# Kernel optimization log

Measured on AMD Instinct MI355X. Metric: run time of the kernel, lower is better.

## Reference

```python
import jax, jax.numpy as jnp
import numpy as np

N = 768      # n_proto (number of class prototypes)
D = 128      # trans_feat_num
H = D // 16  # edge-MLP hidden = 8
A = 312      # semantic attribute dim
INIT_TEMP = 0.1
VTEMP = 10.0
STEMP = 10.0
EPS = 1e-8


def _layer_norm(x, g, b, eps=1e-5):
    m = x.mean(-1, keepdims=True)
    v = ((x - m) ** 2).mean(-1, keepdims=True)
    return (x - m) / jnp.sqrt(v + eps) * g + b


def _instance_norm_rows(x, eps=1e-5):
    # torch InstanceNorm1d on 2D input: unbatched (C, L) -> normalize each row, no affine
    m = x.mean(-1, keepdims=True)
    v = ((x - m) ** 2).mean(-1, keepdims=True)
    return (x - m) / jnp.sqrt(v + eps)


def _init_edge(x, temp):
    # pairwise cosine similarity + row softmax
    nrm = jnp.linalg.norm(x, axis=1)
    sim = (x @ x.T) / jnp.maximum(nrm[:, None] * nrm[None, :], EPS)
    return jax.nn.softmax(sim / temp, axis=-1)


def _edge_update(proto, last_edge, W1, b1, W2, b2, temp):
    n, d = proto.shape
    # O(n^2) pairwise squared differences  -> [n*n, d]
    feat = ((proto[:, None, :] - proto[None, :, :]) ** 2).reshape(n * n, d)
    h = jax.nn.relu(_instance_norm_rows(feat @ W1.T + b1))  # [n*n, H]
    e = jnp.tanh(h @ W2.T + b2).reshape(n, n)
    return jax.nn.softmax(e * (last_edge + EPS) / temp, axis=-1)


def _node_update(proto, last_edge, edge, W, b, g, beta):
    extra = last_edge @ proto          # cross-modal message (dist_injection)
    p = edge @ proto                   # same-modal aggregation
    return jax.nn.relu(_layer_norm((p + extra) @ W.T + b, g, beta)) + p


def setup_inputs() -> dict:
    key = jax.random.key(0)
    ks = jax.random.split(key, 9)
    rn = lambda k, shape, s=1.0: jax.random.normal(k, shape, dtype=jnp.float32) * s
    return {
        "visual_proto": rn(ks[0], (N, D)),
        "semantic_proto": rn(ks[1], (N, D)),
        "attribute": rn(ks[2], (N, A)),
        "Wvn": rn(ks[3], (D, D), 0.08), "bvn": jnp.zeros((D,), jnp.float32),
        "gvn": jnp.ones((D,), jnp.float32), "betavn": jnp.zeros((D,), jnp.float32),
        "Wve1": rn(ks[4], (H, D), 0.1), "bve1": jnp.zeros((H,), jnp.float32),
        "Wve2": rn(ks[5], (1, H), 0.3), "bve2": jnp.zeros((1,), jnp.float32),
        "Wsn": rn(ks[6], (D, D), 0.08), "bsn": jnp.zeros((D,), jnp.float32),
        "gsn": jnp.ones((D,), jnp.float32), "betasn": jnp.zeros((D,), jnp.float32),
        "Wse1": rn(ks[7], (H, D), 0.1), "bse1": jnp.zeros((H,), jnp.float32),
        "Wse2": rn(ks[8], (1, H), 0.3), "bse2": jnp.zeros((1,), jnp.float32),
    }


def reference(visual_proto, semantic_proto, attribute,
              Wvn, bvn, gvn, betavn, Wve1, bve1, Wve2, bve2,
              Wsn, bsn, gsn, betasn, Wse1, bse1, Wse2, bse2):
    ve = _init_edge(visual_proto, INIT_TEMP)
    se = _init_edge(attribute, INIT_TEMP)
    vp = _node_update(visual_proto, se, ve, Wvn, bvn, gvn, betavn)
    ve2 = _edge_update(vp, ve, Wve1, bve1, Wve2, bve2, VTEMP)
    sp = _node_update(semantic_proto, ve2, se, Wsn, bsn, gsn, betasn)
    se2 = _edge_update(sp, se, Wse1, bse1, Wse2, bse2, STEMP)
    return vp, sp, ve2, se2
```

## Files before the change

### kernel.cpp

```cpp
#include <hip/hip_runtime.h>
#include <math.h>

#define NN 768
#define DD 128
#define AA 312
#define HH 8
#define CEPS 1e-8f

typedef __attribute__((ext_vector_type(8))) short s8b;
typedef __attribute__((ext_vector_type(4))) float f4v;

__device__ __forceinline__ float wave_sum(float v) {
    #pragma unroll
    for (int o = 32; o; o >>= 1) v += __shfl_down(v, o, 64);
    return v;
}
__device__ __forceinline__ float wave_max(float v) {
    #pragma unroll
    for (int o = 32; o; o >>= 1) v = fmaxf(v, __shfl_down(v, o, 64));
    return v;
}
__device__ __forceinline__ unsigned short f2bf(float f) {
    unsigned u = __float_as_uint(f);
    u += 0x7FFFu + ((u >> 16) & 1u);
    return (unsigned short)(u >> 16);
}

struct KParams {
    const float *visual, *semantic, *attribute;
    const float *Wvn, *bvn, *gvn, *betavn, *Wve1, *bve1, *Wve2, *bve2;
    const float *Wsn, *bsn, *gsn, *betasn, *Wse1, *bse1, *Wse2, *bse2;
    float *vp, *sp, *ve2, *se2;
    float *simv, *sima, *WvnT, *WsnT, *cvec1, *cvec2;
    float *nrmv, *nrma, *ve, *se;
    short *vpb, *spb;
};

__global__ __launch_bounds__(256) void gram_mfma_kernel(KParams p) {
    __shared__ __align__(16) unsigned short AH[64 * 40];
    __shared__ __align__(16) unsigned short AL[64 * 40];
    __shared__ __align__(16) unsigned short BH[64 * 40];
    __shared__ __align__(16) unsigned short BL[64 * 40];
    const int task = blockIdx.x;
    const int tid = threadIdx.x;
    if (task < 288) {
        const bool isv = (task < 144);
        const int tt = isv ? task : task - 144;
        const int bi = tt / 12, bj = tt % 12;
        const float* M = isv ? p.visual : p.attribute;
        float* G = isv ? p.simv : p.sima;
        float* nrm = isv ? p.nrmv : p.nrma;
        const int K = isv ? DD : AA;
        const int i0 = bi * 64, j0 = bj * 64;
        const int w = tid >> 6, lane = tid & 63;
        const int m = lane & 15, q = lane >> 4;
        f4v acc[4] = {{0.f, 0.f, 0.f, 0.f}, {0.f, 0.f, 0.f, 0.f},
                      {0.f, 0.f, 0.f, 0.f}, {0.f, 0.f, 0.f, 0.f}};
        const int nchunk = (K + 31) >> 5;
        const int srow = tid >> 2, sq = (tid & 3) * 8;
        for (int c = 0; c < nchunk; ++c) {
            const int kc = c * 32;
            __syncthreads();
            #pragma unroll
            for (int h = 0; h < 2; ++h) {
                const int col = sq + h * 4;
                float4 a = {0.f, 0.f, 0.f, 0.f}, b = {0.f, 0.f, 0.f, 0.f};
                if (kc + col + 4 <= K) {
                    a = *(const float4*)(M + (size_t)(i0 + srow) * K + kc + col);
                    b = *(const float4*)(M + (size_t)(j0 + srow) * K + kc + col);
                }
                const float av[4] = {a.x, a.y, a.z, a.w};
                const float bv[4] = {b.x, b.y, b.z, b.w};
                #pragma unroll
                for (int e = 0; e < 4; ++e) {
                    const unsigned short ah = f2bf(av[e]);
                    const float ahf = __uint_as_float((unsigned)ah << 16);
                    const unsigned short al = f2bf(av[e] - ahf);
                    const unsigned short bh = f2bf(bv[e]);
                    const float bhf = __uint_as_float((unsigned)bh << 16);
                    const unsigned short bl = f2bf(bv[e] - bhf);
                    AH[srow * 40 + col + e] = ah;
                    AL[srow * 40 + col + e] = al;
                    BH[srow * 40 + col + e] = bh;
                    BL[srow * 40 + col + e] = bl;
                }
            }
            __syncthreads();
            const s8b ah8 = *(const s8b*)&AH[(w * 16 + m) * 40 + q * 8];
            const s8b al8 = *(const s8b*)&AL[(w * 16 + m) * 40 + q * 8];
            #pragma unroll
            for (int jt = 0; jt < 4; ++jt) {
                const s8b bh8 = *(const s8b*)&BH[(jt * 16 + m) * 40 + q * 8];
                const s8b bl8 = *(const s8b*)&BL[(jt * 16 + m) * 40 + q * 8];
                acc[jt] = __builtin_amdgcn_mfma_f32_16x16x32_bf16(ah8, bh8, acc[jt], 0, 0, 0);
                acc[jt] = __builtin_amdgcn_mfma_f32_16x16x32_bf16(ah8, bl8, acc[jt], 0, 0, 0);
                acc[jt] = __builtin_amdgcn_mfma_f32_16x16x32_bf16(al8, bh8, acc[jt], 0, 0, 0);
            }
        }
        #pragma unroll
        for (int jt = 0; jt < 4; ++jt) {
            #pragma unroll
            for (int r = 0; r < 4; ++r) {
                G[(size_t)(i0 + w * 16 + q * 4 + r) * NN + j0 + jt * 16 + m] = acc[jt][r];
                if (bi == bj && jt == w && m == q * 4 + r)
                    nrm[i0 + w * 16 + m] = sqrtf(fmaxf(acc[jt][r], 0.f));
            }
        }
    } else {
        float* smem = (float*)AH;
        const int u = task - 288;
        const float* S = (u >= 16) ? p.Wsn : p.Wvn;
        float* Dt = (u >= 16) ? p.WsnT : p.WvnT;
        const int tile = u & 15;
        const int c0 = (tile & 3) * 32, r0 = (tile >> 2) * 32;
        const int tx = tid & 31, ty = tid >> 5;
        #pragma unroll
        for (int rr = ty; rr < 32; rr += 8)
            smem[rr * 33 + tx] = S[(size_t)(r0 + rr) * DD + c0 + tx];
        __syncthreads();
        #pragma unroll
        for (int rr = ty; rr < 32; rr += 8)
            Dt[(size_t)(c0 + rr) * DD + r0 + tx] = smem[tx * 33 + rr];
    }
}

__device__ void softmax768_pair(float* A, float* B, int tid, float* red) {
    float* buf = (tid < 256) ? A : B;
    const int st = tid & 255;
    const int g = tid >> 8;
    const int w4 = (tid >> 6) & 3;
    float v0 = buf[st], v1 = buf[st + 256], v2 = buf[st + 512];
    float m = wave_max(fmaxf(fmaxf(v0, v1), v2));
    if ((tid & 63) == 0) red[g * 8 + w4] = m;
    __syncthreads();
    m = fmaxf(fmaxf(red[g * 8], red[g * 8 + 1]), fmaxf(red[g * 8 + 2], red[g * 8 + 3]));
    float e0 = __expf(v0 - m), e1 = __expf(v1 - m), e2 = __expf(v2 - m);
    float sw = wave_sum(e0 + e1 + e2);
    if ((tid & 63) == 0) red[g * 8 + 4 + w4] = sw;
    __syncthreads();
    const float s = red[g * 8 + 4] + red[g * 8 + 5] + red[g * 8 + 6] + red[g * 8 + 7];
    const float inv = 1.f / s;
    buf[st] = e0 * inv;
    buf[st + 256] = e1 * inv;
    buf[st + 512] = e2 * inv;
    __syncthreads();
}

__device__ void norm_rows(float (*buf)[NN], const float* __restrict__ nrm, int i0, int tid) {
    const float n0 = nrm[i0], n1 = nrm[i0 + 1];
    for (int k = tid; k < NN; k += 512) {
        const float nj = nrm[k];
        buf[0][k] = buf[0][k] * 10.f / fmaxf(n0 * nj, CEPS);
        buf[1][k] = buf[1][k] * 10.f / fmaxf(n1 * nj, CEPS);
    }
}

__device__ void node_core(const float* __restrict__ P, float (*ep)[NN], float (*ex)[NN],
                          const float* __restrict__ WT, const float* __restrict__ b,
                          const float* __restrict__ g, const float* __restrict__ beta,
                          float* __restrict__ out, const float* __restrict__ W1e,
                          short* __restrict__ outb, float* __restrict__ cvec, int i0, int tid,
                          float* ppart, float* xpart, float (*qs)[DD], float (*tps)[2][DD],
                          float* red) {
    {
        const int kg = tid >> 6, dp = tid & 63, d0 = dp * 2;
        const float2* P2 = (const float2*)P;
        float a00 = 0.f, a01 = 0.f, a10 = 0.f, a11 = 0.f;
        float b00 = 0.f, b01 = 0.f, b10 = 0.f, b11 = 0.f;
        const int kb = kg * 96;
        #pragma unroll 8
        for (int i = 0; i < 96; ++i) {
            const int k = kb + i;
            const float2 pv = P2[(size_t)k * 64 + dp];
            const float e0 = ep[0][k], e1 = ep[1][k];
            const float f0 = ex[0][k], f1 = ex[1][k];
            a00 = fmaf(e0, pv.x, a00); a01 = fmaf(e0, pv.y, a01);
            a10 = fmaf(e1, pv.x, a10); a11 = fmaf(e1, pv.y, a11);
            b00 = fmaf(f0, pv.x, b00); b01 = fmaf(f0, pv.y, b01);
            b10 = fmaf(f1, pv.x, b10); b11 = fmaf(f1, pv.y, b11);
        }
        float* pp = ppart + kg * 260;
        float* xp = xpart + kg * 260;
        pp[d0] = a00; pp[d0 + 1] = a01; pp[130 + d0] = a10; pp[130 + d0 + 1] = a11;
        xp[d0] = b00; xp[d0 + 1] = b01; xp[130 + d0] = b10; xp[130 + d0 + 1] = b11;
    }
    __syncthreads();
    const int rr = (tid >> 7) & 1, d = tid & 127;
    float preg = 0.f;
    if (tid < 256) {
        float p = 0.f, x = 0.f;
        #pragma unroll
        for (int kk = 0; kk < 8; ++kk) {
            p += ppart[kk * 260 + rr * 130 + d];
            x += xpart[kk * 260 + rr * 130 + d];
        }
        qs[rr][d] = p + x;
        preg = p;
    }
    __syncthreads();
    {
        const int sc = tid >> 8, rr2 = (tid >> 7) & 1;
        float t = (sc == 0) ? b[d] : 0.f;
        const int c0 = sc * 64;
        #pragma unroll 4
        for (int c = c0; c < c0 + 64; ++c) t = fmaf(qs[rr2][c], WT[(size_t)c * DD + d], t);
        tps[sc][rr2][d] = t;
    }
    __syncthreads();
    float tval = 0.f;
    if (tid < 256) tval = tps[0][rr][d] + tps[1][rr][d];
    float sm = wave_sum(tid < 256 ? tval : 0.f);
    if ((tid & 63) == 0) red[tid >> 6] = sm;
    __syncthreads();
    if (tid < 256) tval -= (red[2 * rr] + red[2 * rr + 1]) * (1.f / DD);
    float s2 = wave_sum(tid < 256 ? tval * tval : 0.f);
    if ((tid & 63) == 0) red[8 + (tid >> 6)] = s2;
    __syncthreads();
    if (tid < 256) {
        const float var = (red[8 + 2 * rr] + red[8 + 2 * rr + 1]) * (1.f / DD);
        const float ln = tval * rsqrtf(var + 1e-5f) * g[d] + beta[d];
        const float val = fmaxf(ln, 0.f) + preg;
        out[(size_t)(i0 + rr) * DD + d] = val;
        outb[(size_t)(i0 + rr) * DD + d] = (short)f2bf(val);
        qs[rr][d] = val;
    }
    __syncthreads();
    if (tid < 256) {
        const int row = tid >> 7, r = (tid >> 4) & 7, l16 = tid & 15;
        float ssum = 0.f;
        #pragma unroll
        for (int t = 0; t < 8; ++t) {
            const int k = l16 + 16 * t;
            const float pv = qs[row][k];
            ssum = fmaf(W1e[r * DD + k], pv * pv, ssum);
        }
        #pragma unroll
        for (int o = 8; o; o >>= 1) ssum += __shfl_down(ssum, o, 16);
        if (l16 == 0) cvec[(size_t)(i0 + row) * HH + r] = ssum;
    }
}

__global__ __launch_bounds__(512) void node1_kernel(KParams p) {
    __shared__ __align__(16) float ep[2][NN], ex[2][NN];
    __shared__ __align__(16) float ppart[8 * 260], xpart[8 * 260];
    __shared__ __align__(16) float qs[2][DD], tps[2][2][DD];
    __shared__ float red[16];
    const int i0 = blockIdx.x * 2;
    const int tid = threadIdx.x;
    if (tid < 384) {
        ((float4*)ep)[tid] = ((const float4*)(p.simv + (size_t)i0 * NN))[tid];
        ((float4*)ex)[tid] = ((const float4*)(p.sima + (size_t)i0 * NN))[tid];
    }
    __syncthreads();
    norm_rows(ep, p.nrmv, i0, tid);
    norm_rows(ex, p.nrma, i0, tid);
    __syncthreads();
    softmax768_pair(ep[0], ex[0], tid, red);
    softmax768_pair(ep[1], ex[1], tid, red);
    if (tid < 384) {
        ((float4*)(p.ve + (size_t)i0 * NN))[tid] = ((float4*)ep)[tid];
        ((float4*)(p.se + (size_t)i0 * NN))[tid] = ((float4*)ex)[tid];
    }
    node_core(p.visual, ep, ex, p.WvnT, p.bvn, p.gvn, p.betavn, p.vp, p.Wve1, p.vpb, p.cvec1,
              i0, tid, ppart, xpart, qs, tps, red);
}

__device__ void edge_core(const short* __restrict__ PRb, const float* __restrict__ cvec,
                          const float* __restrict__ W1, const float* __restrict__ b1,
                          const float* __restrict__ W2, const float* __restrict__ b2,
                          float invtemp, int i0, int tid, float (*pi)[DD], float* w1s,
                          short* a_sw, float (*Lv)[NN], float (*Ls)[NN]) {
    const int lane = tid & 63, wave = tid >> 6;
    if (tid < 256) {
        const int t = tid >> 6, m = lane & 15, q2 = lane >> 4;
        const int il = m >> 3, r = m & 7;
        const int kb = t * 32 + q2 * 8;
        s8b av;
        #pragma unroll
        for (int e = 0; e < 8; ++e)
            av[e] = (short)f2bf(pi[il][kb + e] * w1s[r * DD + kb + e]);
        *(s8b*)&a_sw[(t * 64 + lane) * 8] = av;
    }
    __syncthreads();
    s8b af[4];
    #pragma unroll
    for (int t = 0; t < 4; ++t) af[t] = *(const s8b*)&a_sw[(t * 64 + lane) * 8];
    const int q = lane >> 4, n = lane & 15;
    const int rbase = (q & 1) * 4;
    const int il = q >> 1;
    const float4 ci4 = *(const float4*)&cvec[(size_t)(i0 + il) * HH + rbase];
    const float4 b14 = *(const float4*)&b1[rbase];
    const float4 w24 = *(const float4*)&W2[rbase];
    const float b2s = b2[0];
    #pragma unroll
    for (int s = 0; s < 6; ++s) {
        const int j = wave * 96 + s * 16 + n;
        f4v acc = {0.f, 0.f, 0.f, 0.f};
        #pragma unroll
        for (int t = 0; t < 4; ++t) {
            const s8b bf = *(const s8b*)(PRb + (size_t)j * DD + t * 32 + q * 8);
            acc = __builtin_amdgcn_mfma_f32_16x16x32_bf16(af[t], bf, acc, 0, 0, 0);
        }
        const float4 cj = *(const float4*)&cvec[(size_t)j * HH + rbase];
        float z[4];
        z[0] = ci4.x + cj.x - 2.f * acc[0] + b14.x;
        z[1] = ci4.y + cj.y - 2.f * acc[1] + b14.y;
        z[2] = ci4.z + cj.z - 2.f * acc[2] + b14.z;
        z[3] = ci4.w + cj.w - 2.f * acc[3] + b14.w;
        float s1 = z[0] + z[1] + z[2] + z[3];
        float s2 = z[0] * z[0] + z[1] * z[1] + z[2] * z[2] + z[3] * z[3];
        s1 += __shfl_xor(s1, 16, 64);
        s2 += __shfl_xor(s2, 16, 64);
        const float mean = s1 * (1.f / HH);
        const float var = fmaxf(s2 * (1.f / HH) - mean * mean, 0.f);
        const float istd = rsqrtf(var + 1e-5f);
        float a2 = 0.f;
        a2 = fmaf(fmaxf((z[0] - mean) * istd, 0.f), w24.x, a2);
        a2 = fmaf(fmaxf((z[1] - mean) * istd, 0.f), w24.y, a2);
        a2 = fmaf(fmaxf((z[2] - mean) * istd, 0.f), w24.z, a2);
        a2 = fmaf(fmaxf((z[3] - mean) * istd, 0.f), w24.w, a2);
        a2 += __shfl_xor(a2, 16, 64);
        const float tv = tanhf(a2 + b2s);
        const float lv = Lv[il][j];
        if ((q & 1) == 0) Ls[il][j] = tv * (lv + CEPS) * invtemp;
    }
    __syncthreads();
}

__global__ __launch_bounds__(512) void edge_node_kernel(KParams p) {
    __shared__ __align__(16) float pi[2][DD];
    __shared__ __align__(16) float w1s[HH * DD];
    __shared__ __align__(16) short a_sw[4 * 64 * 8];
    __shared__ __align__(16) float Lv[2][NN];
    __shared__ __align__(16) float Ls[2][NN];
    __shared__ __align__(16) float ep[2][NN];
    __shared__ __align__(16) float ppart[8 * 260], xpart[8 * 260];
    __shared__ __align__(16) float qs[2][DD], tps[2][2][DD];
    __shared__ float red[16];
    const int i0 = blockIdx.x * 2;
    const int tid = threadIdx.x;
    if (tid < 256) {
        pi[tid >> 7][tid & 127] = p.vp[(size_t)(i0 + (tid >> 7)) * DD + (tid & 127)];
        ((float4*)w1s)[tid] = ((const float4*)p.Wve1)[tid];
    }
    if (tid < 384) {
        ((float4*)Lv)[tid] = ((const float4*)(p.ve + (size_t)i0 * NN))[tid];
        ((float4*)ep)[tid] = ((const float4*)(p.se + (size_t)i0 * NN))[tid];
    }
    __syncthreads();
    edge_core(p.vpb, p.cvec1, p.Wve1, p.bve1, p.Wve2, p.bve2, 0.1f, i0, tid, pi, w1s, a_sw,
              Lv, Ls);
    softmax768_pair(Ls[0], Ls[1], tid, red);
    if (tid < 384)
        ((float4*)(p.ve2 + (size_t)i0 * NN))[tid] = ((float4*)Ls)[tid];
    node_core(p.semantic, ep, Ls, p.WsnT, p.bsn, p.gsn, p.betasn, p.sp, p.Wse1, p.spb,
              p.cvec2, i0, tid, ppart, xpart, qs, tps, red);
}

__global__ __launch_bounds__(512) void edge2_kernel(KParams p) {
    __shared__ __align__(16) float pi[2][DD];
    __shared__ __align__(16) float w1s[HH * DD];
    __shared__ __align__(16) short a_sw[4 * 64 * 8];
    __shared__ __align__(16) float Lv[2][NN];
    __shared__ __align__(16) float Ls[2][NN];
    __shared__ float red[16];
    const int i0 = blockIdx.x * 2;
    const int tid = threadIdx.x;
    if (tid < 256) {
        pi[tid >> 7][tid & 127] = p.sp[(size_t)(i0 + (tid >> 7)) * DD + (tid & 127)];
        ((float4*)w1s)[tid] = ((const float4*)p.Wse1)[tid];
    }
    if (tid < 384)
        ((float4*)Lv)[tid] = ((const float4*)(p.se + (size_t)i0 * NN))[tid];
    __syncthreads();
    edge_core(p.spb, p.cvec2, p.Wse1, p.bse1, p.Wse2, p.bse2, 0.1f, i0, tid, pi, w1s, a_sw,
              Lv, Ls);
    softmax768_pair(Ls[0], Ls[1], tid, red);
    float* d0 = p.se2 + (size_t)i0 * NN;
    float* d1 = p.se2 + (size_t)(i0 + 1) * NN;
    d0[tid] = Ls[0][tid];
    d1[tid] = Ls[1][tid];
    if (tid < NN - 512) {
        d0[tid + 512] = Ls[0][tid + 512];
        d1[tid + 512] = Ls[1][tid + 512];
    }
}

extern "C" void kernel_launch(void* const* d_in, const int* in_sizes, int n_in, void* d_out,
                              int out_size, void* d_ws, size_t ws_size, hipStream_t stream) {
    KParams kp;
    kp.visual    = (const float*)d_in[0];
    kp.semantic  = (const float*)d_in[1];
    kp.attribute = (const float*)d_in[2];
    kp.Wvn  = (const float*)d_in[3];
    kp.bvn  = (const float*)d_in[4];
    kp.gvn  = (const float*)d_in[5];
    kp.betavn = (const float*)d_in[6];
    kp.Wve1 = (const float*)d_in[7];
    kp.bve1 = (const float*)d_in[8];
    kp.Wve2 = (const float*)d_in[9];
    kp.bve2 = (const float*)d_in[10];
    kp.Wsn  = (const float*)d_in[11];
    kp.bsn  = (const float*)d_in[12];
    kp.gsn  = (const float*)d_in[13];
    kp.betasn = (const float*)d_in[14];
    kp.Wse1 = (const float*)d_in[15];
    kp.bse1 = (const float*)d_in[16];
    kp.Wse2 = (const float*)d_in[17];
    kp.bse2 = (const float*)d_in[18];

    float* out = (float*)d_out;
    kp.vp  = out;
    kp.sp  = out + 98304;
    kp.ve2 = out + 196608;
    kp.se2 = out + 786432;

    float* ws = (float*)d_ws;
    kp.simv  = ws;
    kp.sima  = ws + 589824;
    kp.ve    = ws + 1179648;
    kp.se    = ws + 1769472;
    kp.WvnT  = ws + 2949120;
    kp.WsnT  = ws + 2965504;
    kp.cvec1 = ws + 2981888;
    kp.cvec2 = ws + 2988032;
    kp.vpb   = (short*)(ws + 2994176);
    kp.spb   = (short*)(ws + 3043328);
    kp.nrmv  = ws + 3092480;
    kp.nrma  = ws + 3093248;

    gram_mfma_kernel<<<320, 256, 0, stream>>>(kp);
    node1_kernel<<<NN / 2, 512, 0, stream>>>(kp);
    edge_node_kernel<<<NN / 2, 512, 0, stream>>>(kp);
    edge2_kernel<<<NN / 2, 512, 0, stream>>>(kp);
}
```

Measured before the change: 176.9 us.

## Process one row per block instead of two across node and edge kernels

Each block of the three row-wise kernels now handles a single row rather than a pair, which doubles the grid to 768 blocks. The Wx matvec split goes from 2 to 4 chunks, and a single-row block softmax is added. The aim is more blocks in flight and less shared memory per block, for better occupancy across the 256 CUs. The cost is that each block reads the P matrix and weights again, since they are no longer reused across two rows. Half of the MFMA A-tile rows are also zero-padded, which wastes matrix throughput in the edge kernel.

New measurement: 201.0 us. +13.6%, slower.

```diff
diff --git a/kernel.cpp b/kernel.cpp
--- a/kernel.cpp
+++ b/kernel.cpp
@@ -146,139 +146,150 @@
     __syncthreads();
 }
 
-__device__ void norm_rows(float (*buf)[NN], const float* __restrict__ nrm, int i0, int tid) {
-    const float n0 = nrm[i0], n1 = nrm[i0 + 1];
-    for (int k = tid; k < NN; k += 512) {
-        const float nj = nrm[k];
-        buf[0][k] = buf[0][k] * 10.f / fmaxf(n0 * nj, CEPS);
-        buf[1][k] = buf[1][k] * 10.f / fmaxf(n1 * nj, CEPS);
-    }
-}
-
-__device__ void node_core(const float* __restrict__ P, float (*ep)[NN], float (*ex)[NN],
-                          const float* __restrict__ WT, const float* __restrict__ b,
-                          const float* __restrict__ g, const float* __restrict__ beta,
-                          float* __restrict__ out, const float* __restrict__ W1e,
-                          short* __restrict__ outb, float* __restrict__ cvec, int i0, int tid,
-                          float* ppart, float* xpart, float (*qs)[DD], float (*tps)[2][DD],
-                          float* red) {
+__device__ void block_softmax768(float* buf, int tid, float* red) {
+    const int w = tid >> 6, lane = tid & 63;
+    float v0 = buf[tid];
+    float v1 = (tid < NN - 512) ? buf[tid + 512] : -3.4e38f;
+    float m = wave_max(fmaxf(v0, v1));
+    if (lane == 0) red[w] = m;
+    __syncthreads();
+    m = red[0];
+    #pragma unroll
+    for (int i = 1; i < 8; ++i) m = fmaxf(m, red[i]);
+    float e0 = __expf(v0 - m);
+    float e1 = (tid < NN - 512) ? __expf(v1 - m) : 0.f;
+    float sw = wave_sum(e0 + e1);
+    if (lane == 0) red[8 + w] = sw;
+    __syncthreads();
+    float s = 0.f;
+    #pragma unroll
+    for (int i = 0; i < 8; ++i) s += red[8 + i];
+    const float inv = 1.f / s;
+    buf[tid] = e0 * inv;
+    if (tid < NN - 512) buf[tid + 512] = e1 * inv;
+    __syncthreads();
+}
+
+__device__ void node_core1(const float* __restrict__ P, float* ep, float* ex,
+                           const float* __restrict__ WT, const float* __restrict__ b,
+                           const float* __restrict__ g, const float* __restrict__ beta,
+                           float* __restrict__ out, const float* __restrict__ W1e,
+                           short* __restrict__ outb, float* __restrict__ cvec, int i, int tid,
+                           float* ppart, float* xpart, float* qs, float (*tps)[DD],
+                           float* red) {
     {
         const int kg = tid >> 6, dp = tid & 63, d0 = dp * 2;
         const float2* P2 = (const float2*)P;
-        float a00 = 0.f, a01 = 0.f, a10 = 0.f, a11 = 0.f;
-        float b00 = 0.f, b01 = 0.f, b10 = 0.f, b11 = 0.f;
+        float a0 = 0.f, a1 = 0.f, b0 = 0.f, b1 = 0.f;
         const int kb = kg * 96;
         #pragma unroll 8
-        for (int i = 0; i < 96; ++i) {
-            const int k = kb + i;
+        for (int it = 0; it < 96; ++it) {
+            const int k = kb + it;
             const float2 pv = P2[(size_t)k * 64 + dp];
-            const float e0 = ep[0][k], e1 = ep[1][k];
-            const float f0 = ex[0][k], f1 = ex[1][k];
-            a00 = fmaf(e0, pv.x, a00); a01 = fmaf(e0, pv.y, a01);
-            a10 = fmaf(e1, pv.x, a10); a11 = fmaf(e1, pv.y, a11);
-            b00 = fmaf(f0, pv.x, b00); b01 = fmaf(f0, pv.y, b01);
-            b10 = fmaf(f1, pv.x, b10); b11 = fmaf(f1, pv.y, b11);
-        }
-        float* pp = ppart + kg * 260;
-        float* xp = xpart + kg * 260;
-        pp[d0] = a00; pp[d0 + 1] = a01; pp[130 + d0] = a10; pp[130 + d0 + 1] = a11;
-        xp[d0] = b00; xp[d0 + 1] = b01; xp[130 + d0] = b10; xp[130 + d0 + 1] = b11;
-    }
-    __syncthreads();
-    const int rr = (tid >> 7) & 1, d = tid & 127;
+            const float e0 = ep[k], f0 = ex[k];
+            a0 = fmaf(e0, pv.x, a0); a1 = fmaf(e0, pv.y, a1);
+            b0 = fmaf(f0, pv.x, b0); b1 = fmaf(f0, pv.y, b1);
+        }
+        ppart[kg * 130 + d0] = a0; ppart[kg * 130 + d0 + 1] = a1;
+        xpart[kg * 130 + d0] = b0; xpart[kg * 130 + d0 + 1] = b1;
+    }
+    __syncthreads();
+    const int d = tid & 127;
     float preg = 0.f;
-    if (tid < 256) {
-        float p = 0.f, x = 0.f;
+    if (tid < 128) {
+        float pv = 0.f, xv = 0.f;
         #pragma unroll
         for (int kk = 0; kk < 8; ++kk) {
-            p += ppart[kk * 260 + rr * 130 + d];
-            x += xpart[kk * 260 + rr * 130 + d];
-        }
-        qs[rr][d] = p + x;
-        preg = p;
+            pv += ppart[kk * 130 + d];
+            xv += xpart[kk * 130 + d];
+        }
+        qs[d] = pv + xv;
+        preg = pv;
     }
     __syncthreads();
     {
-        const int sc = tid >> 8, rr2 = (tid >> 7) & 1;
+        const int sc = tid >> 7;
         float t = (sc == 0) ? b[d] : 0.f;
-        const int c0 = sc * 64;
+        const int c0 = sc * 32;
         #pragma unroll 4
-        for (int c = c0; c < c0 + 64; ++c) t = fmaf(qs[rr2][c], WT[(size_t)c * DD + d], t);
-        tps[sc][rr2][d] = t;
+        for (int c = c0; c < c0 + 32; ++c) t = fmaf(qs[c], WT[(size_t)c * DD + d], t);
+        tps[sc][d] = t;
     }
     __syncthreads();
     float tval = 0.f;
-    if (tid < 256) tval = tps[0][rr][d] + tps[1][rr][d];
-    float sm = wave_sum(tid < 256 ? tval : 0.f);
-    if ((tid & 63) == 0) red[tid >> 6] = sm;
-    __syncthreads();
-    if (tid < 256) tval -= (red[2 * rr] + red[2 * rr + 1]) * (1.f / DD);
-    float s2 = wave_sum(tid < 256 ? tval * tval : 0.f);
-    if ((tid & 63) == 0) red[8 + (tid >> 6)] = s2;
-    __syncthreads();
-    if (tid < 256) {
-        const float var = (red[8 + 2 * rr] + red[8 + 2 * rr + 1]) * (1.f / DD);
+    if (tid < 128) tval = tps[0][d] + tps[1][d] + tps[2][d] + tps[3][d];
+    float sm = wave_sum(tid < 128 ? tval : 0.f);
+    if ((tid & 63) == 0 && tid < 128) red[tid >> 6] = sm;
+    __syncthreads();
+    if (tid < 128) tval -= (red[0] + red[1]) * (1.f / DD);
+    float s2 = wave_sum(tid < 128 ? tval * tval : 0.f);
+    if ((tid & 63) == 0 && tid < 128) red[8 + (tid >> 6)] = s2;
+    __syncthreads();
+    if (tid < 128) {
+        const float var = (red[8] + red[9]) * (1.f / DD);
         const float ln = tval * rsqrtf(var + 1e-5f) * g[d] + beta[d];
         const float val = fmaxf(ln, 0.f) + preg;
-        out[(size_t)(i0 + rr) * DD + d] = val;
-        outb[(size_t)(i0 + rr) * DD + d] = (short)f2bf(val);
-        qs[rr][d] = val;
-    }
-    __syncthreads();
-    if (tid < 256) {
-        const int row = tid >> 7, r = (tid >> 4) & 7, l16 = tid & 15;
+        out[(size_t)i * DD + d] = val;
+        outb[(size_t)i * DD + d] = (short)f2bf(val);
+        qs[d] = val;
+    }
+    __syncthreads();
+    if (tid < 128) {
+        const int r = tid >> 4, l16 = tid & 15;
         float ssum = 0.f;
         #pragma unroll
         for (int t = 0; t < 8; ++t) {
             const int k = l16 + 16 * t;
-            const float pv = qs[row][k];
+            const float pv = qs[k];
             ssum = fmaf(W1e[r * DD + k], pv * pv, ssum);
         }
         #pragma unroll
         for (int o = 8; o; o >>= 1) ssum += __shfl_down(ssum, o, 16);
-        if (l16 == 0) cvec[(size_t)(i0 + row) * HH + r] = ssum;
+        if (l16 == 0) cvec[(size_t)i * HH + r] = ssum;
     }
 }
 
 __global__ __launch_bounds__(512) void node1_kernel(KParams p) {
-    __shared__ __align__(16) float ep[2][NN], ex[2][NN];
-    __shared__ __align__(16) float ppart[8 * 260], xpart[8 * 260];
-    __shared__ __align__(16) float qs[2][DD], tps[2][2][DD];
+    __shared__ __align__(16) float ep[NN], ex[NN];
+    __shared__ __align__(16) float ppart[8 * 130], xpart[8 * 130];
+    __shared__ __align__(16) float qs[DD], tps[4][DD];
     __shared__ float red[16];
-    const int i0 = blockIdx.x * 2;
+    const int i = blockIdx.x;
     const int tid = threadIdx.x;
-    if (tid < 384) {
-        ((float4*)ep)[tid] = ((const float4*)(p.simv + (size_t)i0 * NN))[tid];
-        ((float4*)ex)[tid] = ((const float4*)(p.sima + (size_t)i0 * NN))[tid];
-    }
-    __syncthreads();
-    norm_rows(ep, p.nrmv, i0, tid);
-    norm_rows(ex, p.nrma, i0, tid);
-    __syncthreads();
-    softmax768_pair(ep[0], ex[0], tid, red);
-    softmax768_pair(ep[1], ex[1], tid, red);
-    if (tid < 384) {
-        ((float4*)(p.ve + (size_t)i0 * NN))[tid] = ((float4*)ep)[tid];
-        ((float4*)(p.se + (size_t)i0 * NN))[tid] = ((float4*)ex)[tid];
-    }
-    node_core(p.visual, ep, ex, p.WvnT, p.bvn, p.gvn, p.betavn, p.vp, p.Wve1, p.vpb, p.cvec1,
-              i0, tid, ppart, xpart, qs, tps, red);
-}
-
-__device__ void edge_core(const short* __restrict__ PRb, const float* __restrict__ cvec,
-                          const float* __restrict__ W1, const float* __restrict__ b1,
-                          const float* __restrict__ W2, const float* __restrict__ b2,
-                          float invtemp, int i0, int tid, float (*pi)[DD], float* w1s,
-                          short* a_sw, float (*Lv)[NN], float (*Ls)[NN]) {
+    if (tid < 192) ((float4*)ep)[tid] = ((const float4*)(p.simv + (size_t)i * NN))[tid];
+    else if (tid < 384) ((float4*)ex)[tid - 192] = ((const float4*)(p.sima + (size_t)i * NN))[tid - 192];
+    __syncthreads();
+    {
+        const float niv = p.nrmv[i], nia = p.nrma[i];
+        const int k0 = tid, k1 = tid + 512;
+        ep[k0] = ep[k0] * 10.f / fmaxf(niv * p.nrmv[k0], CEPS);
+        ex[k0] = ex[k0] * 10.f / fmaxf(nia * p.nrma[k0], CEPS);
+        if (k1 < NN) {
+            ep[k1] = ep[k1] * 10.f / fmaxf(niv * p.nrmv[k1], CEPS);
+            ex[k1] = ex[k1] * 10.f / fmaxf(nia * p.nrma[k1], CEPS);
+        }
+    }
+    __syncthreads();
+    softmax768_pair(ep, ex, tid, red);
+    if (tid < 192) ((float4*)(p.ve + (size_t)i * NN))[tid] = ((float4*)ep)[tid];
+    else if (tid < 384) ((float4*)(p.se + (size_t)i * NN))[tid - 192] = ((float4*)ex)[tid - 192];
+    node_core1(p.visual, ep, ex, p.WvnT, p.bvn, p.gvn, p.betavn, p.vp, p.Wve1, p.vpb, p.cvec1,
+               i, tid, ppart, xpart, qs, tps, red);
+}
+
+__device__ void edge_core1(const short* __restrict__ PRb, const float* __restrict__ cvec,
+                           const float* __restrict__ b1, const float* __restrict__ W2,
+                           const float* __restrict__ b2, float invtemp, int i, int tid,
+                           float* pi, float* w1s, short* a_sw, float* Lv, float* Ls) {
     const int lane = tid & 63, wave = tid >> 6;
     if (tid < 256) {
         const int t = tid >> 6, m = lane & 15, q2 = lane >> 4;
-        const int il = m >> 3, r = m & 7;
+        const int r = m & 7;
         const int kb = t * 32 + q2 * 8;
         s8b av;
         #pragma unroll
         for (int e = 0; e < 8; ++e)
-            av[e] = (short)f2bf(pi[il][kb + e] * w1s[r * DD + kb + e]);
+            av[e] = (m < 8) ? (short)f2bf(pi[kb + e] * w1s[r * DD + kb + e]) : (short)0;
         *(s8b*)&a_sw[(t * 64 + lane) * 8] = av;
     }
     __syncthreads();
@@ -287,8 +298,7 @@
     for (int t = 0; t < 4; ++t) af[t] = *(const s8b*)&a_sw[(t * 64 + lane) * 8];
     const int q = lane >> 4, n = lane & 15;
     const int rbase = (q & 1) * 4;
-    const int il = q >> 1;
-    const float4 ci4 = *(const float4*)&cvec[(size_t)(i0 + il) * HH + rbase];
+    const float4 ci4 = *(const float4*)&cvec[(size_t)i * HH + rbase];
     const float4 b14 = *(const float4*)&b1[rbase];
     const float4 w24 = *(const float4*)&W2[rbase];
     const float b2s = b2[0];
@@ -321,69 +331,51 @@
         a2 = fmaf(fmaxf((z[3] - mean) * istd, 0.f), w24.w, a2);
         a2 += __shfl_xor(a2, 16, 64);
         const float tv = tanhf(a2 + b2s);
-        const float lv = Lv[il][j];
-        if ((q & 1) == 0) Ls[il][j] = tv * (lv + CEPS) * invtemp;
+        const float lv = Lv[j];
+        if (q == 0) Ls[j] = tv * (lv + CEPS) * invtemp;
     }
     __syncthreads();
 }
 
 __global__ __launch_bounds__(512) void edge_node_kernel(KParams p) {
-    __shared__ __align__(16) float pi[2][DD];
+    __shared__ __align__(16) float pi[DD];
     __shared__ __align__(16) float w1s[HH * DD];
     __shared__ __align__(16) short a_sw[4 * 64 * 8];
-    __shared__ __align__(16) float Lv[2][NN];
-    __shared__ __align__(16) float Ls[2][NN];
-    __shared__ __align__(16) float ep[2][NN];
-    __shared__ __align__(16) float ppart[8 * 260], xpart[8 * 260];
-    __shared__ __align__(16) float qs[2][DD], tps[2][2][DD];
+    __shared__ __align__(16) float Lv[NN], Ls[NN], ep[NN];
+    __shared__ __align__(16) float ppart[8 * 130], xpart[8 * 130];
+    __shared__ __align__(16) float qs[DD], tps[4][DD];
     __shared__ float red[16];
-    const int i0 = blockIdx.x * 2;
+    const int i = blockIdx.x;
     const int tid = threadIdx.x;
-    if (tid < 256) {
-        pi[tid >> 7][tid & 127] = p.vp[(size_t)(i0 + (tid >> 7)) * DD + (tid & 127)];
-        ((float4*)w1s)[tid] = ((const float4*)p.Wve1)[tid];
-    }
-    if (tid < 384) {
-        ((float4*)Lv)[tid] = ((const float4*)(p.ve + (size_t)i0 * NN))[tid];
-        ((float4*)ep)[tid] = ((const float4*)(p.se + (size_t)i0 * NN))[tid];
-    }
-    __syncthreads();
-    edge_core(p.vpb, p.cvec1, p.Wve1, p.bve1, p.Wve2, p.bve2, 0.1f, i0, tid, pi, w1s, a_sw,
-              Lv, Ls);
-    softmax768_pair(Ls[0], Ls[1], tid, red);
-    if (tid < 384)
-        ((float4*)(p.ve2 + (size_t)i0 * NN))[tid] = ((float4*)Ls)[tid];
-    node_core(p.semantic, ep, Ls, p.WsnT, p.bsn, p.gsn, p.betasn, p.sp, p.Wse1, p.spb,
-              p.cvec2, i0, tid, ppart, xpart, qs, tps, red);
+    if (tid < 32) ((float4*)pi)[tid] = ((const float4*)(p.vp + (size_t)i * DD))[tid];
+    if (tid < 256) ((float4*)w1s)[tid] = ((const float4*)p.Wve1)[tid];
+    if (tid < 192) ((float4*)Lv)[tid] = ((const float4*)(p.ve + (size_t)i * NN))[tid];
+    else if (tid < 384) ((float4*)ep)[tid - 192] = ((const float4*)(p.se + (size_t)i * NN))[tid - 192];
+    __syncthreads();
+    edge_core1(p.vpb, p.cvec1, p.bve1, p.Wve2, p.bve2, 0.1f, i, tid, pi, w1s, a_sw, Lv, Ls);
+    block_softmax768(Ls, tid, red);
+    if (tid < 192) ((float4*)(p.ve2 + (size_t)i * NN))[tid] = ((float4*)Ls)[tid];
+    node_core1(p.semantic, ep, Ls, p.WsnT, p.bsn, p.gsn, p.betasn, p.sp, p.Wse1, p.spb,
+               p.cvec2, i, tid, ppart, xpart, qs, tps, red);
 }
 
 __global__ __launch_bounds__(512) void edge2_kernel(KParams p) {
-    __shared__ __align__(16) float pi[2][DD];
+    __shared__ __align__(16) float pi[DD];
     __shared__ __align__(16) float w1s[HH * DD];
     __shared__ __align__(16) short a_sw[4 * 64 * 8];
-    __shared__ __align__(16) float Lv[2][NN];
-    __shared__ __align__(16) float Ls[2][NN];
+    __shared__ __align__(16) float Lv[NN], Ls[NN];
     __shared__ float red[16];
-    const int i0 = blockIdx.x * 2;
+    const int i = blockIdx.x;
     const int tid = threadIdx.x;
-    if (tid < 256) {
-        pi[tid >> 7][tid & 127] = p.sp[(size_t)(i0 + (tid >> 7)) * DD + (tid & 127)];
-        ((float4*)w1s)[tid] = ((const float4*)p.Wse1)[tid];
-    }
-    if (tid < 384)
-        ((float4*)Lv)[tid] = ((const float4*)(p.se + (size_t)i0 * NN))[tid];
-    __syncthreads();
-    edge_core(p.spb, p.cvec2, p.Wse1, p.bse1, p.Wse2, p.bse2, 0.1f, i0, tid, pi, w1s, a_sw,
-              Lv, Ls);
-    softmax768_pair(Ls[0], Ls[1], tid, red);
-    float* d0 = p.se2 + (size_t)i0 * NN;
-    float* d1 = p.se2 + (size_t)(i0 + 1) * NN;
-    d0[tid] = Ls[0][tid];
-    d1[tid] = Ls[1][tid];
-    if (tid < NN - 512) {
-        d0[tid + 512] = Ls[0][tid + 512];
-        d1[tid + 512] = Ls[1][tid + 512];
-    }
+    if (tid < 32) ((float4*)pi)[tid] = ((const float4*)(p.sp + (size_t)i * DD))[tid];
+    if (tid < 256) ((float4*)w1s)[tid] = ((const float4*)p.Wse1)[tid];
+    if (tid < 192) ((float4*)Lv)[tid] = ((const float4*)(p.se + (size_t)i * NN))[tid];
+    __syncthreads();
+    edge_core1(p.spb, p.cvec2, p.bse1, p.Wse2, p.bse2, 0.1f, i, tid, pi, w1s, a_sw, Lv, Ls);
+    block_softmax768(Ls, tid, red);
+    float* d0 = p.se2 + (size_t)i * NN;
+    d0[tid] = Ls[tid];
+    if (tid < NN - 512) d0[tid + 512] = Ls[tid + 512];
 }
 
 extern "C" void kernel_launch(void* const* d_in, const int* in_sizes, int n_in, void* d_out,
@@ -430,7 +422,7 @@
     kp.nrma  = ws + 3093248;
 
     gram_mfma_kernel<<<320, 256, 0, stream>>>(kp);
-    node1_kernel<<<NN / 2, 512, 0, stream>>>(kp);
-    edge_node_kernel<<<NN / 2, 512, 0, stream>>>(kp);
-    edge2_kernel<<<NN / 2, 512, 0, stream>>>(kp);
-}
+    node1_kernel<<<NN, 512, 0, stream>>>(kp);
+    edge_node_kernel<<<NN, 512, 0, stream>>>(kp);
+    edge2_kernel<<<NN, 512, 0, stream>>>(kp);
+}
```

## Move edge@proto aggregations to split-bf16 MFMA GEMM kernels

Applied to the files above, without the earlier changes.

Replaces the per-row-pair FP32 FMA aggregation inside node kernels with separate MFMA GEMM kernels. Edge matrices are stored as hi/lo bf16 pairs and the prototypes as transposed bf16. The pipeline now has separate softmax, aggregation, tail (linear+layernorm) and edge kernels. The aim is to cut the scalar FMA cost of the 768x768x128 products. In exchange it adds launches, workspace traffic, and a GEMM grid of only 12 blocks, and it loses some precision because the prototypes are rounded to bf16.

Result: slower. 291.1 us (+64.5%).

```diff
diff --git a/kernel.cpp b/kernel.cpp
--- a/kernel.cpp
+++ b/kernel.cpp
@@ -33,7 +33,9 @@
     float *vp, *sp, *ve2, *se2;
     float *simv, *sima, *WvnT, *WsnT, *cvec1, *cvec2;
     float *nrmv, *nrma, *ve, *se;
-    short *vpb, *spb;
+    float *pagg1, *xagg1, *pagg2, *xagg2;
+    short *vpb, *spb, *visbT, *sembT;
+    short *veh, *vel, *seh, *sel, *ve2h, *ve2l;
 };
 
 __global__ __launch_bounds__(256) void gram_mfma_kernel(KParams p) {
@@ -106,7 +108,7 @@
                     nrm[i0 + w * 16 + m] = sqrtf(fmaxf(acc[jt][r], 0.f));
             }
         }
-    } else {
+    } else if (task < 320) {
         float* smem = (float*)AH;
         const int u = task - 288;
         const float* S = (u >= 16) ? p.Wsn : p.Wvn;
@@ -121,6 +123,21 @@
         #pragma unroll
         for (int rr = ty; rr < 32; rr += 8)
             Dt[(size_t)(c0 + rr) * DD + r0 + tx] = smem[tx * 33 + rr];
+    } else {
+        const int u = task - 320;
+        const bool isv = (u < 12);
+        const float* src = isv ? p.visual : p.semantic;
+        short* dst = isv ? p.visbT : p.sembT;
+        const int r0 = (isv ? u : u - 12) * 64;
+        for (int e = tid * 4; e < 8192; e += 1024) {
+            const int r = r0 + (e >> 7);
+            const int c = e & 127;
+            const float4 v = *(const float4*)(src + (size_t)r * DD + c);
+            dst[(size_t)(c + 0) * NN + r] = (short)f2bf(v.x);
+            dst[(size_t)(c + 1) * NN + r] = (short)f2bf(v.y);
+            dst[(size_t)(c + 2) * NN + r] = (short)f2bf(v.z);
+            dst[(size_t)(c + 3) * NN + r] = (short)f2bf(v.w);
+        }
     }
 }
 
@@ -155,47 +172,91 @@
     }
 }
 
-__device__ void node_core(const float* __restrict__ P, float (*ep)[NN], float (*ex)[NN],
-                          const float* __restrict__ WT, const float* __restrict__ b,
-                          const float* __restrict__ g, const float* __restrict__ beta,
-                          float* __restrict__ out, const float* __restrict__ W1e,
-                          short* __restrict__ outb, float* __restrict__ cvec, int i0, int tid,
-                          float* ppart, float* xpart, float (*qs)[DD], float (*tps)[2][DD],
-                          float* red) {
-    {
-        const int kg = tid >> 6, dp = tid & 63, d0 = dp * 2;
-        const float2* P2 = (const float2*)P;
-        float a00 = 0.f, a01 = 0.f, a10 = 0.f, a11 = 0.f;
-        float b00 = 0.f, b01 = 0.f, b10 = 0.f, b11 = 0.f;
-        const int kb = kg * 96;
-        #pragma unroll 8
-        for (int i = 0; i < 96; ++i) {
-            const int k = kb + i;
-            const float2 pv = P2[(size_t)k * 64 + dp];
-            const float e0 = ep[0][k], e1 = ep[1][k];
-            const float f0 = ex[0][k], f1 = ex[1][k];
-            a00 = fmaf(e0, pv.x, a00); a01 = fmaf(e0, pv.y, a01);
-            a10 = fmaf(e1, pv.x, a10); a11 = fmaf(e1, pv.y, a11);
-            b00 = fmaf(f0, pv.x, b00); b01 = fmaf(f0, pv.y, b01);
-            b10 = fmaf(f1, pv.x, b10); b11 = fmaf(f1, pv.y, b11);
-        }
-        float* pp = ppart + kg * 260;
-        float* xp = xpart + kg * 260;
-        pp[d0] = a00; pp[d0 + 1] = a01; pp[130 + d0] = a10; pp[130 + d0 + 1] = a11;
-        xp[d0] = b00; xp[d0 + 1] = b01; xp[130 + d0] = b10; xp[130 + d0 + 1] = b11;
-    }
-    __syncthreads();
+__global__ __launch_bounds__(512) void sm1_kernel(KParams p) {
+    __shared__ __align__(16) float ep[2][NN], ex[2][NN];
+    __shared__ float red[16];
+    const int i0 = blockIdx.x * 2;
+    const int tid = threadIdx.x;
+    if (tid < 384) {
+        ((float4*)ep)[tid] = ((const float4*)(p.simv + (size_t)i0 * NN))[tid];
+        ((float4*)ex)[tid] = ((const float4*)(p.sima + (size_t)i0 * NN))[tid];
+    }
+    __syncthreads();
+    norm_rows(ep, p.nrmv, i0, tid);
+    norm_rows(ex, p.nrma, i0, tid);
+    __syncthreads();
+    softmax768_pair(ep[0], ex[0], tid, red);
+    softmax768_pair(ep[1], ex[1], tid, red);
+    if (tid < 384) {
+        ((float4*)(p.ve + (size_t)i0 * NN))[tid] = ((float4*)ep)[tid];
+        ((float4*)(p.se + (size_t)i0 * NN))[tid] = ((float4*)ex)[tid];
+    }
+    #pragma unroll
+    for (int j = 0; j < 3; ++j) {
+        const int e = tid + j * 512;
+        const int row = e / NN, k = e - row * NN;
+        const size_t off = (size_t)(i0 + row) * NN + k;
+        float v = ep[row][k];
+        unsigned short h = f2bf(v);
+        p.veh[off] = (short)h;
+        p.vel[off] = (short)f2bf(v - __uint_as_float((unsigned)h << 16));
+        v = ex[row][k];
+        h = f2bf(v);
+        p.seh[off] = (short)h;
+        p.sel[off] = (short)f2bf(v - __uint_as_float((unsigned)h << 16));
+    }
+}
+
+__global__ __launch_bounds__(512) void agg_kernel(
+        const short* __restrict__ Eh, const short* __restrict__ El,
+        const short* __restrict__ Fh, const short* __restrict__ Fl,
+        const short* __restrict__ PT, float* __restrict__ Pagg, float* __restrict__ Xagg) {
+    const int tid = threadIdx.x, lane = tid & 63, wv = tid >> 6;
+    const int grp = wv >> 2, strip = wv & 3;
+    const short* Ah = grp ? Fh : Eh;
+    const short* Al = grp ? Fl : El;
+    float* Out = grp ? Xagg : Pagg;
+    const int m = lane & 15, q = lane >> 4;
+    const int arow = blockIdx.x * 64 + strip * 16 + m;
+    f4v acc[8] = {{0.f, 0.f, 0.f, 0.f}, {0.f, 0.f, 0.f, 0.f}, {0.f, 0.f, 0.f, 0.f},
+                  {0.f, 0.f, 0.f, 0.f}, {0.f, 0.f, 0.f, 0.f}, {0.f, 0.f, 0.f, 0.f},
+                  {0.f, 0.f, 0.f, 0.f}, {0.f, 0.f, 0.f, 0.f}};
+    for (int kb = 0; kb < NN; kb += 32) {
+        const s8b ah = *(const s8b*)(Ah + (size_t)arow * NN + kb + q * 8);
+        const s8b al = *(const s8b*)(Al + (size_t)arow * NN + kb + q * 8);
+        #pragma unroll
+        for (int nt = 0; nt < 8; ++nt) {
+            const s8b bf = *(const s8b*)(PT + (size_t)(nt * 16 + m) * NN + kb + q * 8);
+            acc[nt] = __builtin_amdgcn_mfma_f32_16x16x32_bf16(ah, bf, acc[nt], 0, 0, 0);
+            acc[nt] = __builtin_amdgcn_mfma_f32_16x16x32_bf16(al, bf, acc[nt], 0, 0, 0);
+        }
+    }
+    const int orow = blockIdx.x * 64 + strip * 16 + q * 4;
+    #pragma unroll
+    for (int nt = 0; nt < 8; ++nt) {
+        #pragma unroll
+        for (int r = 0; r < 4; ++r)
+            Out[(size_t)(orow + r) * DD + nt * 16 + m] = acc[nt][r];
+    }
+}
+
+__global__ __launch_bounds__(512) void tail_kernel(
+        const float* __restrict__ Pagg, const float* __restrict__ Xagg,
+        const float* __restrict__ WT, const float* __restrict__ b,
+        const float* __restrict__ g, const float* __restrict__ beta,
+        float* __restrict__ out, const float* __restrict__ W1e,
+        short* __restrict__ outb, float* __restrict__ cvec) {
+    __shared__ __align__(16) float qs[2][DD], tps[2][2][DD];
+    __shared__ float red[16];
+    const int i0 = blockIdx.x * 2;
+    const int tid = threadIdx.x;
     const int rr = (tid >> 7) & 1, d = tid & 127;
     float preg = 0.f;
     if (tid < 256) {
-        float p = 0.f, x = 0.f;
-        #pragma unroll
-        for (int kk = 0; kk < 8; ++kk) {
-            p += ppart[kk * 260 + rr * 130 + d];
-            x += xpart[kk * 260 + rr * 130 + d];
-        }
-        qs[rr][d] = p + x;
-        preg = p;
+        const float pv = Pagg[(size_t)(i0 + rr) * DD + d];
+        const float xv = Xagg[(size_t)(i0 + rr) * DD + d];
+        qs[rr][d] = pv + xv;
+        preg = pv;
     }
     __syncthreads();
     {
@@ -240,36 +301,11 @@
     }
 }
 
-__global__ __launch_bounds__(512) void node1_kernel(KParams p) {
-    __shared__ __align__(16) float ep[2][NN], ex[2][NN];
-    __shared__ __align__(16) float ppart[8 * 260], xpart[8 * 260];
-    __shared__ __align__(16) float qs[2][DD], tps[2][2][DD];
-    __shared__ float red[16];
-    const int i0 = blockIdx.x * 2;
-    const int tid = threadIdx.x;
-    if (tid < 384) {
-        ((float4*)ep)[tid] = ((const float4*)(p.simv + (size_t)i0 * NN))[tid];
-        ((float4*)ex)[tid] = ((const float4*)(p.sima + (size_t)i0 * NN))[tid];
-    }
-    __syncthreads();
-    norm_rows(ep, p.nrmv, i0, tid);
-    norm_rows(ex, p.nrma, i0, tid);
-    __syncthreads();
-    softmax768_pair(ep[0], ex[0], tid, red);
-    softmax768_pair(ep[1], ex[1], tid, red);
-    if (tid < 384) {
-        ((float4*)(p.ve + (size_t)i0 * NN))[tid] = ((float4*)ep)[tid];
-        ((float4*)(p.se + (size_t)i0 * NN))[tid] = ((float4*)ex)[tid];
-    }
-    node_core(p.visual, ep, ex, p.WvnT, p.bvn, p.gvn, p.betavn, p.vp, p.Wve1, p.vpb, p.cvec1,
-              i0, tid, ppart, xpart, qs, tps, red);
-}
-
 __device__ void edge_core(const short* __restrict__ PRb, const float* __restrict__ cvec,
-                          const float* __restrict__ W1, const float* __restrict__ b1,
-                          const float* __restrict__ W2, const float* __restrict__ b2,
-                          float invtemp, int i0, int tid, float (*pi)[DD], float* w1s,
-                          short* a_sw, float (*Lv)[NN], float (*Ls)[NN]) {
+                          const float* __restrict__ b1, const float* __restrict__ W2,
+                          const float* __restrict__ b2, float invtemp, int i0, int tid,
+                          float (*pi)[DD], float* w1s, short* a_sw, float (*Lv)[NN],
+                          float (*Ls)[NN]) {
     const int lane = tid & 63, wave = tid >> 6;
     if (tid < 256) {
         const int t = tid >> 6, m = lane & 15, q2 = lane >> 4;
@@ -327,15 +363,12 @@
     __syncthreads();
 }
 
-__global__ __launch_bounds__(512) void edge_node_kernel(KParams p) {
+__global__ __launch_bounds__(512) void edge1_kernel(KParams p) {
     __shared__ __align__(16) float pi[2][DD];
     __shared__ __align__(16) float w1s[HH * DD];
     __shared__ __align__(16) short a_sw[4 * 64 * 8];
     __shared__ __align__(16) float Lv[2][NN];
     __shared__ __align__(16) float Ls[2][NN];
-    __shared__ __align__(16) float ep[2][NN];
-    __shared__ __align__(16) float ppart[8 * 260], xpart[8 * 260];
-    __shared__ __align__(16) float qs[2][DD], tps[2][2][DD];
     __shared__ float red[16];
     const int i0 = blockIdx.x * 2;
     const int tid = threadIdx.x;
@@ -343,18 +376,23 @@
         pi[tid >> 7][tid & 127] = p.vp[(size_t)(i0 + (tid >> 7)) * DD + (tid & 127)];
         ((float4*)w1s)[tid] = ((const float4*)p.Wve1)[tid];
     }
-    if (tid < 384) {
+    if (tid < 384)
         ((float4*)Lv)[tid] = ((const float4*)(p.ve + (size_t)i0 * NN))[tid];
-        ((float4*)ep)[tid] = ((const float4*)(p.se + (size_t)i0 * NN))[tid];
-    }
-    __syncthreads();
-    edge_core(p.vpb, p.cvec1, p.Wve1, p.bve1, p.Wve2, p.bve2, 0.1f, i0, tid, pi, w1s, a_sw,
-              Lv, Ls);
+    __syncthreads();
+    edge_core(p.vpb, p.cvec1, p.bve1, p.Wve2, p.bve2, 0.1f, i0, tid, pi, w1s, a_sw, Lv, Ls);
     softmax768_pair(Ls[0], Ls[1], tid, red);
     if (tid < 384)
         ((float4*)(p.ve2 + (size_t)i0 * NN))[tid] = ((float4*)Ls)[tid];
-    node_core(p.semantic, ep, Ls, p.WsnT, p.bsn, p.gsn, p.betasn, p.sp, p.Wse1, p.spb,
-              p.cvec2, i0, tid, ppart, xpart, qs, tps, red);
+    #pragma unroll
+    for (int j = 0; j < 3; ++j) {
+        const int e = tid + j * 512;
+        const int row = e / NN, k = e - row * NN;
+        const size_t off = (size_t)(i0 + row) * NN + k;
+        const float v = Ls[row][k];
+        const unsigned short h = f2bf(v);
+        p.ve2h[off] = (short)h;
+        p.ve2l[off] = (short)f2bf(v - __uint_as_float((unsigned)h << 16));
+    }
 }
 
 __global__ __launch_bounds__(512) void edge2_kernel(KParams p) {
@@ -373,8 +411,7 @@
     if (tid < 384)
         ((float4*)Lv)[tid] = ((const float4*)(p.se + (size_t)i0 * NN))[tid];
     __syncthreads();
-    edge_core(p.spb, p.cvec2, p.Wse1, p.bse1, p.Wse2, p.bse2, 0.1f, i0, tid, pi, w1s, a_sw,
-              Lv, Ls);
+    edge_core(p.spb, p.cvec2, p.bse1, p.Wse2, p.bse2, 0.1f, i0, tid, pi, w1s, a_sw, Lv, Ls);
     softmax768_pair(Ls[0], Ls[1], tid, red);
     float* d0 = p.se2 + (size_t)i0 * NN;
     float* d1 = p.se2 + (size_t)(i0 + 1) * NN;
@@ -420,6 +457,10 @@
     kp.sima  = ws + 589824;
     kp.ve    = ws + 1179648;
     kp.se    = ws + 1769472;
+    kp.pagg1 = ws + 2359296;
+    kp.xagg1 = ws + 2457600;
+    kp.pagg2 = ws + 2555904;
+    kp.xagg2 = ws + 2654208;
     kp.WvnT  = ws + 2949120;
     kp.WsnT  = ws + 2965504;
     kp.cvec1 = ws + 2981888;
@@ -428,9 +469,25 @@
     kp.spb   = (short*)(ws + 3043328);
     kp.nrmv  = ws + 3092480;
     kp.nrma  = ws + 3093248;
-
-    gram_mfma_kernel<<<320, 256, 0, stream>>>(kp);
-    node1_kernel<<<NN / 2, 512, 0, stream>>>(kp);
-    edge_node_kernel<<<NN / 2, 512, 0, stream>>>(kp);
+    kp.visbT = (short*)(ws + 3094016);
+    kp.sembT = (short*)(ws + 3143168);
+    kp.veh   = (short*)(ws + 3192320);
+    kp.vel   = (short*)(ws + 3487232);
+    kp.seh   = (short*)(ws + 3782144);
+    kp.sel   = (short*)(ws + 4077056);
+    kp.ve2h  = (short*)(ws + 4371968);
+    kp.ve2l  = (short*)(ws + 4666880);
+
+    gram_mfma_kernel<<<344, 256, 0, stream>>>(kp);
+    sm1_kernel<<<NN / 2, 512, 0, stream>>>(kp);
+    agg_kernel<<<12, 512, 0, stream>>>(kp.veh, kp.vel, kp.seh, kp.sel, kp.visbT, kp.pagg1,
+                                       kp.xagg1);
+    tail_kernel<<<NN / 2, 512, 0, stream>>>(kp.pagg1, kp.xagg1, kp.WvnT, kp.bvn, kp.gvn,
+                                            kp.betavn, kp.vp, kp.Wve1, kp.vpb, kp.cvec1);
+    edge1_kernel<<<NN / 2, 512, 0, stream>>>(kp);
+    agg_kernel<<<12, 512, 0, stream>>>(kp.seh, kp.sel, kp.ve2h, kp.ve2l, kp.sembT, kp.pagg2,
+                                       kp.xagg2);
+    tail_kernel<<<NN / 2, 512, 0, stream>>>(kp.pagg2, kp.xagg2, kp.WsnT, kp.bsn, kp.gsn,
+                                            kp.betasn, kp.sp, kp.Wse1, kp.spb, kp.cvec2);
     edge2_kernel<<<NN / 2, 512, 0, stream>>>(kp);
 }
```
